# Optimization experiments

Measured on AMD Instinct MI355X. Metric: run time of the kernel, lower is better.

## Reference

```python
import jax, jax.numpy as jnp
import numpy as np

DIM = 192
HEADS = 6
WS = 8          # window_size
N = WS * WS     # tokens per window = 64
CH = DIM // HEADS  # per-head channels = 32


def _l2norm(t, eps=1e-12):
    # torch F.normalize(dim=-1): x / max(||x||_2, eps)
    n = jnp.sqrt(jnp.sum(t * t, axis=-1, keepdims=True))
    return t / jnp.maximum(n, eps)


def setup_inputs() -> dict:
    key = jax.random.key(0)
    ks = jax.random.split(key, 8)
    B, C, H, W = 2, DIM, 256, 256
    x = jax.random.normal(ks[0], (B, C, H, W), dtype=jnp.float32)
    s = 0.02
    w_qkv = jax.random.normal(ks[1], (3 * C, C), dtype=jnp.float32) * s          # 1x1 conv, no bias
    w_dw = jax.random.normal(ks[2], (3 * C, 1, 3, 3), dtype=jnp.float32) * s    # depthwise 3x3, no bias
    temperature = jnp.ones((HEADS, 1, 1), dtype=jnp.float32) / np.sqrt(DIM)
    mlp_w = jax.random.normal(ks[3], (N, N), dtype=jnp.float32) * s             # Linear(N, N)
    mlp_b = jnp.zeros((N,), dtype=jnp.float32)
    proj_w = jax.random.normal(ks[4], (C, C), dtype=jnp.float32) * s            # 1x1 conv, bias=True
    proj_b = jnp.zeros((C,), dtype=jnp.float32)
    return {"x": x, "w_qkv": w_qkv, "w_dw": w_dw, "temperature": temperature,
            "mlp_w": mlp_w, "mlp_b": mlp_b, "proj_w": proj_w, "proj_b": proj_b}


def _attn_forward(x, w_qkv, w_dw, temperature, mlp_w, mlp_b, proj_w, proj_b):
    B, C, H, W = x.shape
    # qkv = dwconv3x3(conv1x1(x)); H,W divisible by WS so check_image_size pad is a no-op
    qkv = jnp.einsum('bchw,oc->bohw', x, w_qkv)
    qkv = jax.lax.conv_general_dilated(
        qkv, w_dw, window_strides=(1, 1), padding=((1, 1), (1, 1)),
        feature_group_count=3 * C,
        dimension_numbers=('NCHW', 'OIHW', 'NCHW'))
    H1, W1 = H // WS, W // WS
    # 'b (z head c) (h1 h) (w1 w) -> z (b h1 w1) head c (h w)'
    t = qkv.reshape(B, 3, HEADS, CH, H1, WS, W1, WS)
    t = t.transpose(1, 0, 4, 6, 2, 3, 5, 7).reshape(3, B * H1 * W1, HEADS, CH, N)
    q, k, v = t[0], t[1], t[2]
    q = _l2norm(q)
    k = _l2norm(k)
    # channel attention: [n, heads, c, c]
    attn = jnp.einsum('nhcx,nhdx->nhcd', q, k) * temperature
    attn = jax.nn.softmax(attn, axis=-1)
    out = jnp.einsum('nhcd,nhdx->nhcx', attn, v)
    # block_mlp gating: GELU(Linear_N(v)) * out  (multiplicative, cs has no 'mlp_add')
    gate = jax.nn.gelu(jnp.einsum('nhcx,yx->nhcy', v, mlp_w) + mlp_b, approximate=False)
    out = out * gate
    # '(b h1 w1) head c (h w) -> b (head c) (h1 h) (w1 w)'
    out = out.reshape(B, H1, W1, HEADS, CH, WS, WS)
    out = out.transpose(0, 3, 4, 1, 5, 2, 6).reshape(B, C, H, W)
    # project_out: 1x1 conv with bias
    out = jnp.einsum('bchw,oc->bohw', out, proj_w) + proj_b[None, :, None, None]
    return out


def reference(x, w_qkv, w_dw, temperature, mlp_w, mlp_b, proj_w, proj_b):
    return _attn_forward(x, w_qkv, w_dw, temperature, mlp_w, mlp_b, proj_w, proj_b)
```

## Files before the change

kernel.cpp:

```cpp
#include <hip/hip_runtime.h>
#include <math.h>

#define CIN   192
#define C3    576
#define HWSZ  65536

__global__ __launch_bounds__(256) void conv1x1_gemm(
    const float* __restrict__ X, const float* __restrict__ Wm,
    float* __restrict__ Y) {
  __shared__ float As[16][68];
  __shared__ float Bs[16][256];
  const int pt = blockIdx.x * 256;
  const int ot = blockIdx.y * 64;
  const int b  = blockIdx.z;
  const int Mout = gridDim.y * 64;
  const float* Xb = X + (size_t)b * CIN * HWSZ;
  float* Yb = Y + (size_t)b * (size_t)Mout * HWSZ;
  const int tid = threadIdx.x;
  const int tx = tid & 15, ty = tid >> 4;
  const int oA = tid >> 2;
  const int kA = (tid & 3) * 4;
  float acc[4][16];
#pragma unroll
  for (int i = 0; i < 4; ++i)
#pragma unroll
    for (int j = 0; j < 16; ++j) acc[i][j] = 0.f;

  for (int k0 = 0; k0 < CIN; k0 += 16) {
    float4 av = *(const float4*)(Wm + (size_t)(ot + oA) * CIN + k0 + kA);
    As[kA + 0][oA] = av.x;
    As[kA + 1][oA] = av.y;
    As[kA + 2][oA] = av.z;
    As[kA + 3][oA] = av.w;
#pragma unroll
    for (int i = 0; i < 4; ++i) {
      const int f4 = tid + 256 * i;
      const int k = f4 >> 6, p4 = f4 & 63;
      *(float4*)&Bs[k][p4 * 4] =
          *(const float4*)(Xb + (size_t)(k0 + k) * HWSZ + pt + p4 * 4);
    }
    __syncthreads();
#pragma unroll
    for (int k = 0; k < 16; ++k) {
      const float4 a4 = *(const float4*)&As[k][ty * 4];
      const float4 b0 = *(const float4*)&Bs[k][tx * 4];
      const float4 b1 = *(const float4*)&Bs[k][64 + tx * 4];
      const float4 b2 = *(const float4*)&Bs[k][128 + tx * 4];
      const float4 b3 = *(const float4*)&Bs[k][192 + tx * 4];
      const float avr[4] = {a4.x, a4.y, a4.z, a4.w};
      const float bvr[16] = {b0.x, b0.y, b0.z, b0.w,
                             b1.x, b1.y, b1.z, b1.w,
                             b2.x, b2.y, b2.z, b2.w,
                             b3.x, b3.y, b3.z, b3.w};
#pragma unroll
      for (int i = 0; i < 4; ++i)
#pragma unroll
        for (int j = 0; j < 16; ++j) acc[i][j] += avr[i] * bvr[j];
    }
    __syncthreads();
  }
#pragma unroll
  for (int i = 0; i < 4; ++i) {
    const int o = ot + ty * 4 + i;
#pragma unroll
    for (int j4 = 0; j4 < 4; ++j4) {
      float4 r;
      r.x = acc[i][j4 * 4 + 0];
      r.y = acc[i][j4 * 4 + 1];
      r.z = acc[i][j4 * 4 + 2];
      r.w = acc[i][j4 * 4 + 3];
      *(float4*)(Yb + (size_t)o * HWSZ + pt + j4 * 64 + tx * 4) = r;
    }
  }
}

__global__ __launch_bounds__(256) void dwconv_win(
    const float* __restrict__ qkv, const float* __restrict__ wdw,
    float* __restrict__ Bw, int gbase) {
  __shared__ float t[10][264];
  const int gc = blockIdx.x;
  const int h1 = blockIdx.y;
  const int b  = blockIdx.z;
  const int tid = threadIdx.x;
  const int r0 = h1 * 8 - 1;
  const float* src = qkv + ((size_t)b * 192 + gc) * HWSZ;

  for (int idx = tid; idx < 640; idx += 256) {
    const int row = idx >> 6, cv = idx & 63;
    const int gr = r0 + row;
    float4 v = make_float4(0.f, 0.f, 0.f, 0.f);
    if ((unsigned)gr < 256u) v = *(const float4*)(src + gr * 256 + cv * 4);
    *(float4*)&t[row][4 + cv * 4] = v;
  }
  if (tid < 10) { t[tid][3] = 0.f; t[tid][260] = 0.f; }
  __syncthreads();

  const float* w9 = wdw + (size_t)(gbase + gc) * 9;
  const float w0 = w9[0], w1 = w9[1], w2 = w9[2];
  const float w3 = w9[3], w4 = w9[4], w5 = w9[5];
  const float w6 = w9[6], w7 = w9[7], w8 = w9[8];

  const int c = tid;
  const int wv = c >> 3, tt = c & 7;
  float* rec = Bw + (((size_t)(b * 1024 + h1 * 32 + wv) * C3) + gbase + gc) * 64
               + tt;

  float x0 = t[0][c + 3], x1 = t[0][c + 4], x2 = t[0][c + 5];
  float y0 = t[1][c + 3], y1 = t[1][c + 4], y2 = t[1][c + 5];
#pragma unroll
  for (int rr = 1; rr <= 8; ++rr) {
    const float z0 = t[rr + 1][c + 3], z1 = t[rr + 1][c + 4],
                z2 = t[rr + 1][c + 5];
    const float res = x0 * w0 + x1 * w1 + x2 * w2
                    + y0 * w3 + y1 * w4 + y2 * w5
                    + z0 * w6 + z1 * w7 + z2 * w8;
    rec[(rr - 1) * 8] = res;
    x0 = y0; x1 = y1; x2 = y2;
    y0 = z0; y1 = z1; y2 = z2;
  }
}

__global__ __launch_bounds__(256) void gate_gemm(
    const float* __restrict__ Bw, const float* __restrict__ mlpw,
    const float* __restrict__ mlpb, float* __restrict__ gate) {
  __shared__ float VT[64 * 68];
  __shared__ float WT[64 * 68];
  const int blk = blockIdx.x;
  const int rec = blk / 3;
  const int sub = blk - rec * 3;
  const int tid = threadIdx.x;

  const float* vsrc = Bw + (size_t)rec * (C3 * 64) + (384 + sub * 64) * 64;
#pragma unroll
  for (int i = 0; i < 4; ++i) {
    const int f4 = tid + 256 * i;
    const int r = f4 >> 4, x0 = (f4 & 15) * 4;
    const float4 v = *(const float4*)(vsrc + r * 64 + x0);
    VT[(x0 + 0) * 68 + r] = v.x;
    VT[(x0 + 1) * 68 + r] = v.y;
    VT[(x0 + 2) * 68 + r] = v.z;
    VT[(x0 + 3) * 68 + r] = v.w;
    const float4 w = *(const float4*)(mlpw + r * 64 + x0);
    WT[(x0 + 0) * 68 + r] = w.x;
    WT[(x0 + 1) * 68 + r] = w.y;
    WT[(x0 + 2) * 68 + r] = w.z;
    WT[(x0 + 3) * 68 + r] = w.w;
  }
  __syncthreads();

  const int tx = tid & 15, ty = tid >> 4;
  float acc[4][4];
#pragma unroll
  for (int i = 0; i < 4; ++i)
#pragma unroll
    for (int j = 0; j < 4; ++j) acc[i][j] = 0.f;

  for (int x = 0; x < 64; ++x) {
    const float4 a4 = *(const float4*)&VT[x * 68 + ty * 4];
    const float4 b4 = *(const float4*)&WT[x * 68 + tx * 4];
    const float avr[4] = {a4.x, a4.y, a4.z, a4.w};
    const float bvr[4] = {b4.x, b4.y, b4.z, b4.w};
#pragma unroll
    for (int i = 0; i < 4; ++i)
#pragma unroll
      for (int j = 0; j < 4; ++j) acc[i][j] += avr[i] * bvr[j];
  }

  const float kE = 0.70710678118654752f;
  const float b0 = mlpb[tx * 4 + 0], b1 = mlpb[tx * 4 + 1];
  const float b2 = mlpb[tx * 4 + 2], b3 = mlpb[tx * 4 + 3];
#pragma unroll
  for (int i = 0; i < 4; ++i) {
    const int row = ty * 4 + i;
    float g0 = acc[i][0] + b0;
    float g1 = acc[i][1] + b1;
    float g2 = acc[i][2] + b2;
    float g3 = acc[i][3] + b3;
    g0 = 0.5f * g0 * (1.f + erff(g0 * kE));
    g1 = 0.5f * g1 * (1.f + erff(g1 * kE));
    g2 = 0.5f * g2 * (1.f + erff(g2 * kE));
    g3 = 0.5f * g3 * (1.f + erff(g3 * kE));
    float* dst = gate + ((size_t)rec * 192 + sub * 64 + row) * 64 + tx * 4;
    *(float4*)dst = make_float4(g0, g1, g2, g3);
  }
}

__global__ __launch_bounds__(256, 5) void attn_bw2(
    const float* __restrict__ Bw, const float* __restrict__ temp,
    float* __restrict__ yw) {
  __shared__ float dwv[64 * 97];
  __shared__ float attnS[32 * 33];
  __shared__ float scl[64];
  const int bid = blockIdx.x;
  const int b   = bid / 6144;
  const int rr  = bid % 6144;
  const int xcd = rr & 7;
  const int s   = rr >> 3;
  const int head = s % 6;
  const int wloc = s / 6;
  const int win  = xcd * 128 + wloc;
  const int tid = threadIdx.x;
  const int ch = tid >> 3;
  const int iy = tid & 7;

  {
    const float* rec = Bw + (size_t)(b * 1024 + win) * C3 * 64;
    const int t8 = iy * 8;
#pragma unroll
    for (int g = 0; g < 3; ++g) {
      const float* sp = rec + (size_t)(g * 192 + head * 32 + ch) * 64 + t8;
      const float4 v0 = *(const float4*)sp;
      const float4 v1 = *(const float4*)(sp + 4);
      const int gc = g * 32 + ch;
      dwv[(t8 + 0) * 97 + gc] = v0.x;
      dwv[(t8 + 1) * 97 + gc] = v0.y;
      dwv[(t8 + 2) * 97 + gc] = v0.z;
      dwv[(t8 + 3) * 97 + gc] = v0.w;
      dwv[(t8 + 4) * 97 + gc] = v1.x;
      dwv[(t8 + 5) * 97 + gc] = v1.y;
      dwv[(t8 + 6) * 97 + gc] = v1.z;
      dwv[(t8 + 7) * 97 + gc] = v1.w;
    }
  }
  __syncthreads();

  if (tid < 64) {
    float ss = 0.f;
    for (int t = 0; t < 64; ++t) {
      const float v = dwv[t * 97 + tid];
      ss += v * v;
    }
    scl[tid] = 1.f / fmaxf(sqrtf(ss), 1e-12f);
  }
  __syncthreads();

  {
    const int c = tid >> 3, m = tid & 7;
    float sa[4] = {0.f, 0.f, 0.f, 0.f};
    for (int t = 0; t < 64; ++t) {
      const float qv = dwv[t * 97 + c];
#pragma unroll
      for (int j = 0; j < 4; ++j) sa[j] += qv * dwv[t * 97 + 32 + m * 4 + j];
    }
    const float qs = scl[c] * temp[head];
#pragma unroll
    for (int j = 0; j < 4; ++j) sa[j] *= qs * scl[32 + m * 4 + j];
    float mx = fmaxf(fmaxf(sa[0], sa[1]), fmaxf(sa[2], sa[3]));
    for (int off = 1; off < 8; off <<= 1) mx = fmaxf(mx, __shfl_xor(mx, off, 8));
    float sum = 0.f;
#pragma unroll
    for (int j = 0; j < 4; ++j) {
      sa[j] = expf(sa[j] - mx);
      sum += sa[j];
    }
    for (int off = 1; off < 8; off <<= 1) sum += __shfl_xor(sum, off, 8);
    const float inv = 1.f / sum;
#pragma unroll
    for (int j = 0; j < 4; ++j) attnS[c * 33 + m * 4 + j] = sa[j] * inv;
  }
  __syncthreads();

  {
    const int c = ch;
    float* dst = yw + (((size_t)(b * 1024 + win) * 192 + head * 32 + c) * 64
                       + iy * 8);
    const float4 gA = *(const float4*)dst;
    const float4 gB = *(const float4*)(dst + 4);
    float ov[8] = {0.f, 0.f, 0.f, 0.f, 0.f, 0.f, 0.f, 0.f};
    const int tb = iy * 8 * 97 + 64;
    for (int d = 0; d < 32; ++d) {
      const float a = attnS[c * 33 + d];
#pragma unroll
      for (int j = 0; j < 8; ++j) ov[j] += a * dwv[tb + j * 97 + d];
    }
    *(float4*)dst       = make_float4(ov[0] * gA.x, ov[1] * gA.y,
                                      ov[2] * gA.z, ov[3] * gA.w);
    *(float4*)(dst + 4) = make_float4(ov[4] * gB.x, ov[5] * gB.y,
                                      ov[6] * gB.z, ov[7] * gB.w);
  }
}

__global__ __launch_bounds__(256) void proj_gemm(
    const float* __restrict__ yw, const float* __restrict__ Wm,
    const float* __restrict__ bias, float* __restrict__ out) {
  __shared__ float As[16][68];
  __shared__ float Bs[16][256];
  const int ptile = blockIdx.x;
  const int ot = blockIdx.y * 64;
  const int b  = blockIdx.z;
  const int h1 = ptile >> 3, w4 = ptile & 7;
  const int win0 = h1 * 32 + w4 * 4;
  const int tid = threadIdx.x;
  const int tx = tid & 15, ty = tid >> 4;
  const int oA = tid >> 2, kA = (tid & 3) * 4;
  float acc[4][16];
#pragma unroll
  for (int i = 0; i < 4; ++i)
#pragma unroll
    for (int j = 0; j < 16; ++j) acc[i][j] = 0.f;

  const float* ywb = yw + (size_t)(b * 1024 + win0) * 192 * 64;
  for (int k0 = 0; k0 < 192; k0 += 16) {
    float4 av = *(const float4*)(Wm + (size_t)(ot + oA) * 192 + k0 + kA);
    As[kA + 0][oA] = av.x;
    As[kA + 1][oA] = av.y;
    As[kA + 2][oA] = av.z;
    As[kA + 3][oA] = av.w;
#pragma unroll
    for (int i = 0; i < 4; ++i) {
      const int f4 = tid + 256 * i;
      const int k = f4 >> 6, p4 = f4 & 63;
      const int wv = p4 >> 4, tt = (p4 & 15) * 4;
      *(float4*)&Bs[k][p4 * 4] =
          *(const float4*)(ywb + ((size_t)wv * 192 + k0 + k) * 64 + tt);
    }
    __syncthreads();
#pragma unroll
    for (int k = 0; k < 16; ++k) {
      const float4 a4 = *(const float4*)&As[k][ty * 4];
      const float4 b0 = *(const float4*)&Bs[k][tx * 4];
      const float4 b1 = *(const float4*)&Bs[k][64 + tx * 4];
      const float4 b2 = *(const float4*)&Bs[k][128 + tx * 4];
      const float4 b3 = *(const float4*)&Bs[k][192 + tx * 4];
      const float avr[4] = {a4.x, a4.y, a4.z, a4.w};
      const float bvr[16] = {b0.x, b0.y, b0.z, b0.w,
                             b1.x, b1.y, b1.z, b1.w,
                             b2.x, b2.y, b2.z, b2.w,
                             b3.x, b3.y, b3.z, b3.w};
#pragma unroll
      for (int i = 0; i < 4; ++i)
#pragma unroll
        for (int j = 0; j < 16; ++j) acc[i][j] += avr[i] * bvr[j];
    }
    __syncthreads();
  }
  const int colbase = w4 * 32;
#pragma unroll
  for (int i = 0; i < 4; ++i) {
    const int o = ot + ty * 4 + i;
    const float bv = bias[o];
    float* ob = out + ((size_t)(b * 192 + o) * 256 + h1 * 8) * 256 + colbase;
#pragma unroll
    for (int j = 0; j < 16; ++j) {
      const int p = (j >> 2) * 64 + tx * 4 + (j & 3);
      const int wv = p >> 6;
      const int t = p & 63;
      ob[(t >> 3) * 256 + wv * 8 + (t & 7)] = acc[i][j] + bv;
    }
  }
}

extern "C" void kernel_launch(void* const* d_in, const int* in_sizes, int n_in,
                              void* d_out, int out_size, void* d_ws, size_t ws_size,
                              hipStream_t stream) {
  const float* x           = (const float*)d_in[0];
  const float* w_qkv       = (const float*)d_in[1];
  const float* w_dw        = (const float*)d_in[2];
  const float* temperature = (const float*)d_in[3];
  const float* mlp_w       = (const float*)d_in[4];
  const float* mlp_b       = (const float*)d_in[5];
  const float* proj_w      = (const float*)d_in[6];
  const float* proj_b      = (const float*)d_in[7];
  float* out = (float*)d_out;

  float* slice = (float*)d_ws;
  float* Bw    = slice + (size_t)2 * 192 * HWSZ;

  for (int g = 0; g < 3; ++g) {
    conv1x1_gemm<<<dim3(256, 3, 2), 256, 0, stream>>>(
        x, w_qkv + (size_t)g * 192 * CIN, slice);
    dwconv_win<<<dim3(192, 32, 2), 256, 0, stream>>>(
        slice, w_dw, Bw, g * 192);
  }
  gate_gemm<<<dim3(6144), 256, 0, stream>>>(Bw, mlp_w, mlp_b, slice);
  attn_bw2<<<dim3(12288), 256, 0, stream>>>(Bw, temperature, slice);
  proj_gemm<<<dim3(256, 3, 2), 256, 0, stream>>>(slice, proj_w, proj_b, out);
}
```

Baseline: 947.8 us.

## Use split-bf16 MFMA for the qkv 1x1 conv GEMM

Replaces the FP32 FMA tiled GEMM for the qkv 1x1 convolution with a kernel built on MFMA 16x16x32 bf16 instructions. Each FP32 operand is split into a high and a low bf16 part, and three MFMA products (hh, hl, lh) are accumulated to recover near-FP32 accuracy. The change targets the FP32 ALU cost of the GEMM. In exchange it adds conversion work, scalar strided global loads of X instead of float4 loads, and scalar uncoalesced output stores, and accuracy is slightly below true FP32.

New measurement: 803.6 us. -15.2%, faster.

```diff
diff --git a/kernel.cpp b/kernel.cpp
--- a/kernel.cpp
+++ b/kernel.cpp
@@ -5,11 +5,26 @@
 #define C3    576
 #define HWSZ  65536
 
-__global__ __launch_bounds__(256) void conv1x1_gemm(
+typedef __attribute__((ext_vector_type(8))) short bf16x8;
+typedef __attribute__((ext_vector_type(4))) float f32x4;
+
+__device__ inline void cvt_hilo(float x, short& hi, short& lo) {
+  union { float f; unsigned u; } a; a.f = x;
+  unsigned hb = (a.u + 0x7FFFu + ((a.u >> 16) & 1u)) & 0xFFFF0000u;
+  hi = (short)(hb >> 16);
+  union { unsigned u; float f; } h; h.u = hb;
+  float r = x - h.f;
+  union { float f; unsigned u; } c; c.f = r;
+  lo = (short)((c.u + 0x7FFFu + ((c.u >> 16) & 1u)) >> 16);
+}
+
+__global__ __launch_bounds__(256) void conv1x1_mfma(
     const float* __restrict__ X, const float* __restrict__ Wm,
     float* __restrict__ Y) {
-  __shared__ float As[16][68];
-  __shared__ float Bs[16][256];
+  __shared__ short Ah[4][64][8];
+  __shared__ short Al[4][64][8];
+  __shared__ short Bh[16][64][8];
+  __shared__ short Bl[16][64][8];
   const int pt = blockIdx.x * 256;
   const int ot = blockIdx.y * 64;
   const int b  = blockIdx.z;
@@ -17,61 +32,86 @@
   const float* Xb = X + (size_t)b * CIN * HWSZ;
   float* Yb = Y + (size_t)b * (size_t)Mout * HWSZ;
   const int tid = threadIdx.x;
-  const int tx = tid & 15, ty = tid >> 4;
-  const int oA = tid >> 2;
-  const int kA = (tid & 3) * 4;
-  float acc[4][16];
-#pragma unroll
-  for (int i = 0; i < 4; ++i)
-#pragma unroll
-    for (int j = 0; j < 16; ++j) acc[i][j] = 0.f;
-
-  for (int k0 = 0; k0 < CIN; k0 += 16) {
-    float4 av = *(const float4*)(Wm + (size_t)(ot + oA) * CIN + k0 + kA);
-    As[kA + 0][oA] = av.x;
-    As[kA + 1][oA] = av.y;
-    As[kA + 2][oA] = av.z;
-    As[kA + 3][oA] = av.w;
-#pragma unroll
-    for (int i = 0; i < 4; ++i) {
-      const int f4 = tid + 256 * i;
-      const int k = f4 >> 6, p4 = f4 & 63;
-      *(float4*)&Bs[k][p4 * 4] =
-          *(const float4*)(Xb + (size_t)(k0 + k) * HWSZ + pt + p4 * 4);
-    }
+  const int lane = tid & 63;
+  const int wave = tid >> 6;
+
+  f32x4 acc[4][4];
+#pragma unroll
+  for (int j = 0; j < 4; ++j)
+#pragma unroll
+    for (int m = 0; m < 4; ++m) acc[j][m] = (f32x4){0.f, 0.f, 0.f, 0.f};
+
+  for (int k0 = 0; k0 < CIN; k0 += 32) {
     __syncthreads();
-#pragma unroll
-    for (int k = 0; k < 16; ++k) {
-      const float4 a4 = *(const float4*)&As[k][ty * 4];
-      const float4 b0 = *(const float4*)&Bs[k][tx * 4];
-      const float4 b1 = *(const float4*)&Bs[k][64 + tx * 4];
-      const float4 b2 = *(const float4*)&Bs[k][128 + tx * 4];
-      const float4 b3 = *(const float4*)&Bs[k][192 + tx * 4];
-      const float avr[4] = {a4.x, a4.y, a4.z, a4.w};
-      const float bvr[16] = {b0.x, b0.y, b0.z, b0.w,
-                             b1.x, b1.y, b1.z, b1.w,
-                             b2.x, b2.y, b2.z, b2.w,
-                             b3.x, b3.y, b3.z, b3.w};
-#pragma unroll
-      for (int i = 0; i < 4; ++i)
-#pragma unroll
-        for (int j = 0; j < 16; ++j) acc[i][j] += avr[i] * bvr[j];
+    {
+      const int wt = tid >> 6, l = tid & 63;
+      const int o = ot + wt * 16 + (l & 15);
+      const int kk = k0 + (l >> 4) * 8;
+      const float4 w0 = *(const float4*)(Wm + (size_t)o * CIN + kk);
+      const float4 w1 = *(const float4*)(Wm + (size_t)o * CIN + kk + 4);
+      const float wv[8] = {w0.x, w0.y, w0.z, w0.w, w1.x, w1.y, w1.z, w1.w};
+      short hv[8], lv[8];
+#pragma unroll
+      for (int j = 0; j < 8; ++j) cvt_hilo(wv[j], hv[j], lv[j]);
+      *(bf16x8*)(&Ah[wt][l][0]) =
+          (bf16x8){hv[0], hv[1], hv[2], hv[3], hv[4], hv[5], hv[6], hv[7]};
+      *(bf16x8*)(&Al[wt][l][0]) =
+          (bf16x8){lv[0], lv[1], lv[2], lv[3], lv[4], lv[5], lv[6], lv[7]};
+    }
+#pragma unroll
+    for (int q = 0; q < 4; ++q) {
+      const int flg = q * 256 + tid;
+      const int n = flg >> 6, l = flg & 63;
+      const int p = pt + n * 16 + (l & 15);
+      const int kk = k0 + (l >> 4) * 8;
+      float xv[8];
+#pragma unroll
+      for (int j = 0; j < 8; ++j) xv[j] = Xb[(size_t)(kk + j) * HWSZ + p];
+      short hv[8], lv[8];
+#pragma unroll
+      for (int j = 0; j < 8; ++j) cvt_hilo(xv[j], hv[j], lv[j]);
+      *(bf16x8*)(&Bh[n][l][0]) =
+          (bf16x8){hv[0], hv[1], hv[2], hv[3], hv[4], hv[5], hv[6], hv[7]};
+      *(bf16x8*)(&Bl[n][l][0]) =
+          (bf16x8){lv[0], lv[1], lv[2], lv[3], lv[4], lv[5], lv[6], lv[7]};
     }
     __syncthreads();
-  }
-#pragma unroll
-  for (int i = 0; i < 4; ++i) {
-    const int o = ot + ty * 4 + i;
-#pragma unroll
-    for (int j4 = 0; j4 < 4; ++j4) {
-      float4 r;
-      r.x = acc[i][j4 * 4 + 0];
-      r.y = acc[i][j4 * 4 + 1];
-      r.z = acc[i][j4 * 4 + 2];
-      r.w = acc[i][j4 * 4 + 3];
-      *(float4*)(Yb + (size_t)o * HWSZ + pt + j4 * 64 + tx * 4) = r;
-    }
-  }
+
+    bf16x8 bh[4], bl[4];
+#pragma unroll
+    for (int m = 0; m < 4; ++m) {
+      bh[m] = *(const bf16x8*)(&Bh[wave * 4 + m][lane][0]);
+      bl[m] = *(const bf16x8*)(&Bl[wave * 4 + m][lane][0]);
+    }
+#pragma unroll
+    for (int j = 0; j < 4; ++j) {
+      const bf16x8 ah = *(const bf16x8*)(&Ah[j][lane][0]);
+      const bf16x8 al = *(const bf16x8*)(&Al[j][lane][0]);
+#pragma unroll
+      for (int m = 0; m < 4; ++m) {
+        acc[j][m] = __builtin_amdgcn_mfma_f32_16x16x32_bf16(ah, bh[m],
+                                                            acc[j][m], 0, 0, 0);
+        acc[j][m] = __builtin_amdgcn_mfma_f32_16x16x32_bf16(ah, bl[m],
+                                                            acc[j][m], 0, 0, 0);
+        acc[j][m] = __builtin_amdgcn_mfma_f32_16x16x32_bf16(al, bh[m],
+                                                            acc[j][m], 0, 0, 0);
+      }
+    }
+  }
+
+  const int row0 = (lane >> 4) * 4;
+  const int col  = lane & 15;
+#pragma unroll
+  for (int j = 0; j < 4; ++j)
+#pragma unroll
+    for (int m = 0; m < 4; ++m) {
+#pragma unroll
+      for (int r = 0; r < 4; ++r) {
+        const int o = ot + j * 16 + row0 + r;
+        const int p = pt + (wave * 4 + m) * 16 + col;
+        Yb[(size_t)o * HWSZ + p] = acc[j][m][r];
+      }
+    }
 }
 
 __global__ __launch_bounds__(256) void dwconv_win(
@@ -367,7 +407,7 @@
   float* Bw    = slice + (size_t)2 * 192 * HWSZ;
 
   for (int g = 0; g < 3; ++g) {
-    conv1x1_gemm<<<dim3(256, 3, 2), 256, 0, stream>>>(
+    conv1x1_mfma<<<dim3(256, 3, 2), 256, 0, stream>>>(
         x, w_qkv + (size_t)g * 192 * CIN, slice);
     dwconv_win<<<dim3(192, 32, 2), 256, 0, stream>>>(
         slice, w_dw, Bw, g * 192);
```
